# Kernel optimization log

Measured on AMD Instinct MI355X. Metric: run time of the kernel, lower is better.

## Reference

```python
import jax, jax.numpy as jnp
import numpy as np

B, S, D = 32, 128, 1024      # encoder batch, seq len, embed_dim
C = 65536                    # nclasses (sense inventory)
N = 512                      # number of gathered WSD target tokens
NNZ = 262144                 # nnz of sparse label adjacency A (avg degree 4)
EPS = 1e-5                   # BatchNorm1d eps


def setup_inputs() -> dict:
    key = jax.random.key(0)
    ks = jax.random.split(key, 7)
    enc_out = jax.random.normal(ks[0], (B, S, D), dtype=jnp.float32)
    batch_idx = jax.random.randint(ks[1], (N,), 0, B)
    tgt = jax.random.randint(ks[2], (N,), 0, S)
    A_indices = jax.random.randint(ks[3], (2, NNZ), 0, C)
    A_values = jax.random.uniform(ks[4], (NNZ,), dtype=jnp.float32)
    wt2_w = jax.random.normal(ks[5], (C, D), dtype=jnp.float32) / np.sqrt(D).astype(np.float32)
    wt2_b = jax.random.normal(ks[6], (C,), dtype=jnp.float32) * 0.02
    return {"enc_out": enc_out, "wt2_w": wt2_w, "wt2_b": wt2_b,
            "A_values": A_values, "batch_idx": batch_idx, "tgt": tgt,
            "A_indices": A_indices}


def reference(enc_out, wt2_w, wt2_b, A_values, batch_idx, tgt, A_indices):
    # gather target-token embeddings: [N, D]
    g = enc_out[batch_idx, tgt]
    # BatchNorm1d(affine=False), training mode -> batch stats, biased var
    mean = jnp.mean(g, axis=0)
    var = jnp.var(g, axis=0)
    h0 = (g - mean) / jnp.sqrt(var + EPS)
    # wt2 Linear + swish -> logits over classes Z: [N, C]
    h1 = jax.nn.swish(h0 @ wt2_w.T + wt2_b)
    # sparse spmm: torch_sparse.spmm(ii, vv, m=C, n=C, matrix=Z.T).T == Z @ A.T
    row, col = A_indices[0], A_indices[1]
    gathered = h1.T[col] * A_values[:, None]            # [NNZ, N]
    neighbors = jax.ops.segment_sum(gathered, row, num_segments=C).T  # [N, C]
    # residual add (renormalize=False)
    return neighbors + h1
```

## Files before the change

### kernel.cpp

```cpp
#include <hip/hip_runtime.h>
#include <hip/hip_bf16.h>

typedef unsigned short u16;
typedef unsigned int   u32;
typedef __attribute__((ext_vector_type(8))) short bf16x8;
typedef __attribute__((ext_vector_type(4))) float f32x4;

static constexpr int kS = 128, kD = 1024, kC = 65536, kN = 512, kNNZ = 262144;

__device__ __forceinline__ u16 f2bf(float x) {
  u32 u = __float_as_uint(x);
  u32 r = (u + 0x7fffu + ((u >> 16) & 1u)) >> 16;
  return (u16)r;
}
__device__ __forceinline__ u32 pack2(float a, float b) {
  return (u32)f2bf(a) | ((u32)f2bf(b) << 16);
}
__device__ __forceinline__ float bf_lo(u32 v) { return __uint_as_float(v << 16); }
__device__ __forceinline__ float bf_hi(u32 v) { return __uint_as_float(v & 0xffff0000u); }

__global__ void k_bn_part(const float* __restrict__ enc, const int* __restrict__ bidx,
                          const int* __restrict__ tgt, float* __restrict__ part) {
  __shared__ int offs[64];
  int n0 = blockIdx.y * 64;
  if (threadIdx.x < 64) offs[threadIdx.x] = bidx[n0 + threadIdx.x] * kS + tgt[n0 + threadIdx.x];
  __syncthreads();
  int d = blockIdx.x * 256 + threadIdx.x;
  float s = 0.f, ss = 0.f;
  for (int i = 0; i < 64; ++i) {
    float v = enc[(size_t)offs[i] * kD + d];
    s += v; ss += v * v;
  }
  part[(blockIdx.y * 2 + 0) * kD + d] = s;
  part[(blockIdx.y * 2 + 1) * kD + d] = ss;
}

__global__ void k_bn_fin(const float* __restrict__ part, float* __restrict__ mean,
                         float* __restrict__ rstd) {
  int d = blockIdx.x * 256 + threadIdx.x;
  float s = 0.f, ss = 0.f;
#pragma unroll
  for (int b = 0; b < 8; ++b) {
    s  += part[(b * 2 + 0) * kD + d];
    ss += part[(b * 2 + 1) * kD + d];
  }
  float m = s * (1.f / kN);
  float var = ss * (1.f / kN) - m * m;
  mean[d] = m;
  rstd[d] = 1.f / sqrtf(var + 1e-5f);
}

__global__ void k_bn_pack(const float* __restrict__ enc, const int* __restrict__ bidx,
                          const int* __restrict__ tgt, const float* __restrict__ mean,
                          const float* __restrict__ rstd, u16* __restrict__ Bp) {
  int i = blockIdx.x * 256 + threadIdx.x;
  int n = i & 511;
  int g = i >> 9;
  int k0 = g * 8;
  size_t src = (size_t)(bidx[n] * kS + tgt[n]) * kD + k0;
  float4 v0 = *(const float4*)(enc + src);
  float4 v1 = *(const float4*)(enc + src + 4);
  float4 m0 = *(const float4*)(mean + k0);
  float4 m1 = *(const float4*)(mean + k0 + 4);
  float4 r0 = *(const float4*)(rstd + k0);
  float4 r1 = *(const float4*)(rstd + k0 + 4);
  u32 q0 = pack2((v0.x - m0.x) * r0.x, (v0.y - m0.y) * r0.y);
  u32 q1 = pack2((v0.z - m0.z) * r0.z, (v0.w - m0.w) * r0.w);
  u32 q2 = pack2((v1.x - m1.x) * r1.x, (v1.y - m1.y) * r1.y);
  u32 q3 = pack2((v1.z - m1.z) * r1.z, (v1.w - m1.w) * r1.w);
  *(uint4*)(Bp + (size_t)i * 8) = make_uint4(q0, q1, q2, q3);
}

__global__ void k_hist(const int* __restrict__ rows, int* __restrict__ hist) {
  int e = blockIdx.x * blockDim.x + threadIdx.x;
  if (e < kNNZ) atomicAdd(&hist[rows[e]], 1);
}

__global__ __launch_bounds__(1024) void k_scan(int* __restrict__ hist, int* __restrict__ cursor) {
  __shared__ int sm[1024];
  int t = threadIdx.x;
  int base = t * 64;
  int sum = 0;
  for (int i = 0; i < 64; ++i) sum += hist[base + i];
  sm[t] = sum;
  __syncthreads();
  for (int off = 1; off < 1024; off <<= 1) {
    int v = (t >= off) ? sm[t - off] : 0;
    __syncthreads();
    sm[t] += v;
    __syncthreads();
  }
  int run = sm[t] - sum;
  for (int i = 0; i < 64; ++i) {
    int v = hist[base + i];
    hist[base + i] = run;
    cursor[base + i] = run;
    run += v;
  }
  if (t == 1023) hist[kC] = run;
}

__global__ void k_scatter(const int* __restrict__ rows, const int* __restrict__ cols,
                          const float* __restrict__ vals, int* __restrict__ cursor,
                          int* __restrict__ scol, float* __restrict__ sval) {
  int e = blockIdx.x * blockDim.x + threadIdx.x;
  if (e < kNNZ) {
    int r = rows[e];
    int p = atomicAdd(&cursor[r], 1);
    scol[p] = cols[e];
    sval[p] = vals[e];
  }
}

__global__ __launch_bounds__(1024)
void k_gemm_f2(const float* __restrict__ W, const u16* __restrict__ Bp,
               const float* __restrict__ bias, u16* __restrict__ h1t) {
  __shared__ __align__(16) u16 Ab0[128 * 36];
  __shared__ __align__(16) u16 Ab1[128 * 36];
  const int t = threadIdx.x;
  const int l = t & 63;
  const int w = t >> 6;
  const int wm = (w >> 3) * 64, wn = (w & 7) * 64;
  const int cb = blockIdx.x * 128;
  const int ar = t >> 3, aq = t & 7;
  const int q = l >> 4, ln = l & 15;
  const float* gA = W + (size_t)(cb + ar) * kD + aq * 4;
  u16* awp0 = Ab0 + ar * 36 + aq * 4;
  u16* awp1 = Ab1 + ar * 36 + aq * 4;
  const u16* gB = Bp + ((size_t)q * 512 + wn + ln) * 8;

  f32x4 acc[4][4];
#pragma unroll
  for (int a = 0; a < 4; ++a)
#pragma unroll
    for (int b = 0; b < 4; ++b) acc[a][b] = (f32x4){0.f, 0.f, 0.f, 0.f};

  float4 fA;
  bf16x8 bvA[4], bvB[4];

  fA = *(const float4*)(gA);
#pragma unroll
  for (int nb = 0; nb < 4; ++nb) bvA[nb] = *(const bf16x8*)(gB + nb * 128);
  *(uint2*)awp0 = make_uint2(pack2(fA.x, fA.y), pack2(fA.z, fA.w));
  fA = *(const float4*)(gA + 32);
#pragma unroll
  for (int nb = 0; nb < 4; ++nb) bvB[nb] = *(const bf16x8*)(gB + 16384 + nb * 128);
  asm volatile("s_waitcnt lgkmcnt(0)" ::: "memory");
  __builtin_amdgcn_s_barrier();
  __builtin_amdgcn_sched_barrier(0);

#pragma unroll 1
  for (int tt = 0; tt < 16; ++tt) {
    {
#pragma unroll
      for (int mb = 0; mb < 4; ++mb) {
        bf16x8 af = *(const bf16x8*)(Ab0 + (wm + mb * 16 + ln) * 36 + q * 8);
#pragma unroll
        for (int nb = 0; nb < 4; ++nb)
          acc[mb][nb] = __builtin_amdgcn_mfma_f32_16x16x32_bf16(af, bvA[nb], acc[mb][nb], 0, 0, 0);
      }
      *(uint2*)awp1 = make_uint2(pack2(fA.x, fA.y), pack2(fA.z, fA.w));
      int ktn = (2 * tt + 2) & 31;
      fA = *(const float4*)(gA + ktn * 32);
#pragma unroll
      for (int nb = 0; nb < 4; ++nb)
        bvA[nb] = *(const bf16x8*)(gB + (size_t)ktn * 16384 + nb * 128);
      asm volatile("s_waitcnt lgkmcnt(0)" ::: "memory");
      __builtin_amdgcn_s_barrier();
      __builtin_amdgcn_sched_barrier(0);
    }
    {
#pragma unroll
      for (int mb = 0; mb < 4; ++mb) {
        bf16x8 af = *(const bf16x8*)(Ab1 + (wm + mb * 16 + ln) * 36 + q * 8);
#pragma unroll
        for (int nb = 0; nb < 4; ++nb)
          acc[mb][nb] = __builtin_amdgcn_mfma_f32_16x16x32_bf16(af, bvB[nb], acc[mb][nb], 0, 0, 0);
      }
      if (tt < 15) {
        *(uint2*)awp0 = make_uint2(pack2(fA.x, fA.y), pack2(fA.z, fA.w));
        int ktn = 2 * tt + 3;
        fA = *(const float4*)(gA + ktn * 32);
#pragma unroll
        for (int nb = 0; nb < 4; ++nb)
          bvB[nb] = *(const bf16x8*)(gB + (size_t)ktn * 16384 + nb * 128);
        asm volatile("s_waitcnt lgkmcnt(0)" ::: "memory");
        __builtin_amdgcn_s_barrier();
        __builtin_amdgcn_sched_barrier(0);
      }
    }
  }

#pragma unroll
  for (int mb = 0; mb < 4; ++mb) {
    int rb = wm + mb * 16 + q * 4;
#pragma unroll
    for (int i = 0; i < 4; ++i) {
      int c = cb + rb + i;
      float bvs = bias[c];
#pragma unroll
      for (int nb = 0; nb < 4; ++nb) {
        float x = acc[mb][nb][i] + bvs;
        float sw = x / (1.f + __expf(-x));
        h1t[(size_t)c * kN + (wn + nb * 16 + ln)] = f2bf(sw);
      }
    }
  }
}

__global__ __launch_bounds__(512)
void k_spmm(const u16* __restrict__ h1t, const int* __restrict__ rowptr,
            const int* __restrict__ scol, const float* __restrict__ sval,
            float* __restrict__ out) {
  __shared__ float tile[32 * 512];
  int r0 = blockIdx.x * 32;
  int t = threadIdx.x, w = t >> 6, l = t & 63;
#pragma unroll
  for (int j = 0; j < 4; ++j) {
    int rl = w * 4 + j;
    int r = r0 + rl;
    uint4 hv = ((const uint4*)(h1t + (size_t)r * kN))[l];
    float a0 = bf_lo(hv.x), a1 = bf_hi(hv.x), a2 = bf_lo(hv.y), a3 = bf_hi(hv.y);
    float a4 = bf_lo(hv.z), a5 = bf_hi(hv.z), a6 = bf_lo(hv.w), a7 = bf_hi(hv.w);
    int e0 = rowptr[r], e1 = rowptr[r + 1];
    int c = 0; float v = 0.f;
    if (e0 < e1) { c = scol[e0]; v = sval[e0]; }
    for (int e = e0; e < e1; ++e) {
      uint4 cv = ((const uint4*)(h1t + (size_t)c * kN))[l];
      int cn = 0; float vn = 0.f;
      if (e + 1 < e1) { cn = scol[e + 1]; vn = sval[e + 1]; }
      a0 = fmaf(v, bf_lo(cv.x), a0); a1 = fmaf(v, bf_hi(cv.x), a1);
      a2 = fmaf(v, bf_lo(cv.y), a2); a3 = fmaf(v, bf_hi(cv.y), a3);
      a4 = fmaf(v, bf_lo(cv.z), a4); a5 = fmaf(v, bf_hi(cv.z), a5);
      a6 = fmaf(v, bf_lo(cv.w), a6); a7 = fmaf(v, bf_hi(cv.w), a7);
      c = cn; v = vn;
    }
    int sw = (rl & 7) << 2;
    *(float4*)&tile[rl * 512 + ((8 * l) ^ sw)]     = make_float4(a0, a1, a2, a3);
    *(float4*)&tile[rl * 512 + ((8 * l + 4) ^ sw)] = make_float4(a4, a5, a6, a7);
  }
  __syncthreads();
  int r = l & 31;
  int swr = (r & 7) << 2;
#pragma unroll
  for (int it = 0; it < 32; ++it) {
    int n = it * 16 + w * 2 + (l >> 5);
    out[(size_t)n * kC + r0 + r] = tile[r * 512 + (n ^ swr)];
  }
}

extern "C" void kernel_launch(void* const* d_in, const int* in_sizes, int n_in,
                              void* d_out, int out_size, void* d_ws, size_t ws_size,
                              hipStream_t stream) {
  (void)in_sizes; (void)n_in; (void)out_size; (void)ws_size;
  const float* enc   = (const float*)d_in[0];
  const float* W     = (const float*)d_in[1];
  const float* bias  = (const float*)d_in[2];
  const float* Avals = (const float*)d_in[3];
  const int*   bidx  = (const int*)d_in[4];
  const int*   tgt   = (const int*)d_in[5];
  const int*   Arow  = (const int*)d_in[6];
  const int*   Acol  = Arow + kNNZ;
  float* out = (float*)d_out;

  char* ws = (char*)d_ws;
  float* mean   = (float*)(ws);
  float* rstd   = (float*)(ws + 4096);
  u16*   Bp     = (u16*)  (ws + 8192);
  int*   rowptr = (int*)  (ws + 1056768);
  int*   cursor = (int*)  (ws + 1319168);
  int*   scol   = (int*)  (ws + 1581312);
  float* sval   = (float*)(ws + 2629888);
  float* part   = (float*)(ws + 3678464);
  u16*   h1t    = (u16*)  (ws + 4194304);

  hipMemsetAsync(rowptr, 0, (kC + 1) * sizeof(int), stream);
  k_bn_part<<<dim3(4, 8), 256, 0, stream>>>(enc, bidx, tgt, part);
  k_bn_fin<<<4, 256, 0, stream>>>(part, mean, rstd);
  k_bn_pack<<<256, 256, 0, stream>>>(enc, bidx, tgt, mean, rstd, Bp);
  k_hist<<<kNNZ / 256, 256, 0, stream>>>(Arow, rowptr);
  k_scan<<<1, 1024, 0, stream>>>(rowptr, cursor);
  k_scatter<<<kNNZ / 256, 256, 0, stream>>>(Arow, Acol, Avals, cursor, scol, sval);
  k_gemm_f2<<<kC / 128, 1024, 0, stream>>>(W, Bp, bias, h1t);
  k_spmm<<<kC / 32, 512, 0, stream>>>(h1t, rowptr, scol, sval, out);
}
```

Measured before the change: 285.6 us.

## Shrink GEMM tile to 64 rows with 512 threads and double-buffer spmm gathers

The GEMM kernel now uses 64-row class tiles with 8 waves of 512 threads. Each wave covers all 64 rows and a 64-column slice of N, and launch bounds now request 4 blocks per CU for more occupancy and more blocks to spread over the CUs. The W-to-LDS staging (t>>3 rows) now matches 64 rows. The spmm inner loop keeps two neighbour-row gathers in flight at once, to hide gather latency rather than prefetching only indices. The cost is that each Bp tile is loaded twice as often per class row, and the accumulator tiles add register pressure.

```diff
diff --git a/kernel.cpp b/kernel.cpp
--- a/kernel.cpp
+++ b/kernel.cpp
@@ -112,16 +112,16 @@
   }
 }
 
-__global__ __launch_bounds__(1024)
-void k_gemm_f2(const float* __restrict__ W, const u16* __restrict__ Bp,
+__global__ __launch_bounds__(512, 4)
+void k_gemm_f3(const float* __restrict__ W, const u16* __restrict__ Bp,
                const float* __restrict__ bias, u16* __restrict__ h1t) {
-  __shared__ __align__(16) u16 Ab0[128 * 36];
-  __shared__ __align__(16) u16 Ab1[128 * 36];
+  __shared__ __align__(16) u16 Ab0[64 * 36];
+  __shared__ __align__(16) u16 Ab1[64 * 36];
   const int t = threadIdx.x;
   const int l = t & 63;
   const int w = t >> 6;
-  const int wm = (w >> 3) * 64, wn = (w & 7) * 64;
-  const int cb = blockIdx.x * 128;
+  const int wn = w * 64;
+  const int cb = blockIdx.x * 64;
   const int ar = t >> 3, aq = t & 7;
   const int q = l >> 4, ln = l & 15;
   const float* gA = W + (size_t)(cb + ar) * kD + aq * 4;
@@ -154,7 +154,7 @@
     {
 #pragma unroll
       for (int mb = 0; mb < 4; ++mb) {
-        bf16x8 af = *(const bf16x8*)(Ab0 + (wm + mb * 16 + ln) * 36 + q * 8);
+        bf16x8 af = *(const bf16x8*)(Ab0 + (mb * 16 + ln) * 36 + q * 8);
 #pragma unroll
         for (int nb = 0; nb < 4; ++nb)
           acc[mb][nb] = __builtin_amdgcn_mfma_f32_16x16x32_bf16(af, bvA[nb], acc[mb][nb], 0, 0, 0);
@@ -172,7 +172,7 @@
     {
 #pragma unroll
       for (int mb = 0; mb < 4; ++mb) {
-        bf16x8 af = *(const bf16x8*)(Ab1 + (wm + mb * 16 + ln) * 36 + q * 8);
+        bf16x8 af = *(const bf16x8*)(Ab1 + (mb * 16 + ln) * 36 + q * 8);
 #pragma unroll
         for (int nb = 0; nb < 4; ++nb)
           acc[mb][nb] = __builtin_amdgcn_mfma_f32_16x16x32_bf16(af, bvB[nb], acc[mb][nb], 0, 0, 0);
@@ -193,7 +193,7 @@
 
 #pragma unroll
   for (int mb = 0; mb < 4; ++mb) {
-    int rb = wm + mb * 16 + q * 4;
+    int rb = mb * 16 + q * 4;
 #pragma unroll
     for (int i = 0; i < 4; ++i) {
       int c = cb + rb + i;
@@ -207,6 +207,12 @@
     }
   }
 }
+
+#define FMA8(cv, v)                                                        \
+  a0 = fmaf(v, bf_lo(cv.x), a0); a1 = fmaf(v, bf_hi(cv.x), a1);            \
+  a2 = fmaf(v, bf_lo(cv.y), a2); a3 = fmaf(v, bf_hi(cv.y), a3);            \
+  a4 = fmaf(v, bf_lo(cv.z), a4); a5 = fmaf(v, bf_hi(cv.z), a5);            \
+  a6 = fmaf(v, bf_lo(cv.w), a6); a7 = fmaf(v, bf_hi(cv.w), a7);
 
 __global__ __launch_bounds__(512)
 void k_spmm(const u16* __restrict__ h1t, const int* __restrict__ rowptr,
@@ -223,17 +229,29 @@
     float a0 = bf_lo(hv.x), a1 = bf_hi(hv.x), a2 = bf_lo(hv.y), a3 = bf_hi(hv.y);
     float a4 = bf_lo(hv.z), a5 = bf_hi(hv.z), a6 = bf_lo(hv.w), a7 = bf_hi(hv.w);
     int e0 = rowptr[r], e1 = rowptr[r + 1];
-    int c = 0; float v = 0.f;
-    if (e0 < e1) { c = scol[e0]; v = sval[e0]; }
-    for (int e = e0; e < e1; ++e) {
-      uint4 cv = ((const uint4*)(h1t + (size_t)c * kN))[l];
-      int cn = 0; float vn = 0.f;
-      if (e + 1 < e1) { cn = scol[e + 1]; vn = sval[e + 1]; }
-      a0 = fmaf(v, bf_lo(cv.x), a0); a1 = fmaf(v, bf_hi(cv.x), a1);
-      a2 = fmaf(v, bf_lo(cv.y), a2); a3 = fmaf(v, bf_hi(cv.y), a3);
-      a4 = fmaf(v, bf_lo(cv.z), a4); a5 = fmaf(v, bf_hi(cv.z), a5);
-      a6 = fmaf(v, bf_lo(cv.w), a6); a7 = fmaf(v, bf_hi(cv.w), a7);
-      c = cn; v = vn;
+    uint4 cv0 = {}, cv1 = {};
+    float v0 = 0.f, v1 = 0.f;
+    if (e0 < e1) {
+      v0 = sval[e0];
+      cv0 = ((const uint4*)(h1t + (size_t)scol[e0] * kN))[l];
+    }
+    if (e0 + 1 < e1) {
+      v1 = sval[e0 + 1];
+      cv1 = ((const uint4*)(h1t + (size_t)scol[e0 + 1] * kN))[l];
+    }
+    for (int e = e0; e < e1; e += 2) {
+      FMA8(cv0, v0);
+      if (e + 2 < e1) {
+        v0 = sval[e + 2];
+        cv0 = ((const uint4*)(h1t + (size_t)scol[e + 2] * kN))[l];
+      }
+      if (e + 1 < e1) {
+        FMA8(cv1, v1);
+        if (e + 3 < e1) {
+          v1 = sval[e + 3];
+          cv1 = ((const uint4*)(h1t + (size_t)scol[e + 3] * kN))[l];
+        }
+      }
     }
     int sw = (rl & 7) << 2;
     *(float4*)&tile[rl * 512 + ((8 * l) ^ sw)]     = make_float4(a0, a1, a2, a3);
@@ -281,6 +299,6 @@
   k_hist<<<kNNZ / 256, 256, 0, stream>>>(Arow, rowptr);
   k_scan<<<1, 1024, 0, stream>>>(rowptr, cursor);
   k_scatter<<<kNNZ / 256, 256, 0, stream>>>(Arow, Acol, Avals, cursor, scol, sval);
-  k_gemm_f2<<<kC / 128, 1024, 0, stream>>>(W, Bp, bias, h1t);
+  k_gemm_f3<<<kC / 64, 512, 0, stream>>>(W, Bp, bias, h1t);
   k_spmm<<<kC / 32, 512, 0, stream>>>(h1t, rowptr, scol, sval, out);
 }
```

Measured after the change: 292.9 us. 1.03x slower.
